# Performance work log

Measured on AMD Instinct MI355X. Metric: run time of the kernel, lower is better.

The kernel has to match this reference:

```python
import jax, jax.numpy as jnp
import numpy as np

B, T, D, U = 64, 512, 256, 512


def setup_inputs() -> dict:
    key = jax.random.key(0)
    ks = jax.random.split(key, 8)
    g = lambda k, shape: (jax.random.normal(k, shape, dtype=jnp.float32) * 0.05)
    return {
        "x": jax.random.normal(ks[0], (B, T, D), dtype=jnp.float32),
        "h0": jnp.zeros((B, U), jnp.float32),
        "c0": jnp.zeros((B, U), jnp.float32),
        "W_f_short": g(ks[1], (D + U, U)),
        "b_f_short": -jnp.ones((U,), jnp.float32),
        "W_f_long": g(ks[2], (D + U, U)),
        "b_f_long": jnp.ones((U,), jnp.float32),
        "W_alpha": g(ks[3], (D + U, U)),
        "b_alpha": jnp.zeros((U,), jnp.float32),
        "W_m": g(ks[4], (D + U, D)),
        "b_m": jnp.zeros((D,), jnp.float32),
        "W_C": g(ks[5], (D + U, U)),
        "b_C": jnp.zeros((U,), jnp.float32),
        "W_o": g(ks[6], (D + U, U)),
        "b_o": jnp.zeros((U,), jnp.float32),
    }


def reference(x, h0, c0, W_f_short, b_f_short, W_f_long, b_f_long,
              W_alpha, b_alpha, W_m, b_m, W_C, b_C, W_o, b_o):
    # Fuse the five matmuls that share the same input hx=[h_prev, x_t]
    # into one; W_C uses a different input (hxm) and stays separate.
    units = h0.shape[-1]
    d = x.shape[-1]
    W_cat = jnp.concatenate([W_f_short, W_f_long, W_alpha, W_o, W_m], axis=1)
    b_cat = jnp.concatenate([b_f_short, b_f_long, b_alpha, b_o, b_m], axis=0)
    splits = np.cumsum([units, units, units, units])[:-0 or None]

    def step(carry, x_t):
        h_prev, c_prev = carry
        hx = jnp.concatenate([h_prev, x_t], axis=-1)          # [B, U+D]
        gates = hx @ W_cat + b_cat                            # [B, 4U+D]
        f_short = jax.nn.sigmoid(gates[:, :units])
        f_long = jax.nn.sigmoid(gates[:, units:2 * units])
        alpha = jax.nn.sigmoid(gates[:, 2 * units:3 * units])
        o_t = jax.nn.sigmoid(gates[:, 3 * units:4 * units])
        m_t = jax.nn.sigmoid(gates[:, 4 * units:])            # [B, D]
        f_t = alpha * f_short + (1.0 - alpha) * f_long
        i_t = 1.0 - f_t
        mod_x = m_t * x_t
        hxm = jnp.concatenate([h_prev, mod_x], axis=-1)
        c_hat = jnp.tanh(hxm @ W_C + b_C)
        c_t = f_t * c_prev + i_t * c_hat
        h_t = o_t * jnp.tanh(c_t)
        return (h_t, c_t), h_t

    xs = jnp.swapaxes(x, 0, 1)                                # [T, B, D]
    (_, _), hs = jax.lax.scan(step, (h0, c0), xs)             # hs: [T, B, U]
    return jnp.swapaxes(hs, 0, 1)                             # [B, T, U]
```

## Files before the change

### kernel.cpp

```cpp
#include <hip/hip_runtime.h>
#include <hip/hip_fp16.h>
#include <math.h>

typedef _Float16 h2 __attribute__((ext_vector_type(2)));
typedef _Float16 h8 __attribute__((ext_vector_type(8)));
typedef float    f4 __attribute__((ext_vector_type(4)));
typedef unsigned short     u16;
typedef unsigned int       u32;
typedef unsigned long long u64;

#define BB 64
#define TT 512
#define DD 256
#define UU 512

#define NBLK 64
#define CPB  44
#define XPB  36
#define UPB  8
#define MPB  4
#define NJ   2816
#define NJX  2304

#define OFF_W1   0ull
#define OFF_W2   (OFF_W1 + 2816ull*512*2)
#define OFF_WX   (OFF_W2 + 512ull*256*2)
#define OFF_B1   (OFF_WX + 2304ull*256*2)
#define OFF_HB   (OFF_B1 + 2816ull*4)
#define OFF_MX   (OFF_HB + 64ull*512*2)
#define OFF_CTR  (OFF_MX + 64ull*256*2)
#define OFF_XPRE (OFF_CTR + 16400ull*4)
#define WS_FULL  (OFF_XPRE + 512ull*2304*64*2)

__device__ __forceinline__ float sigf(float v)     { return 1.0f / (1.0f + __expf(-v)); }
__device__ __forceinline__ float tanhfast(float v) { return 1.0f - 2.0f / (__expf(2.0f * v) + 1.0f); }

__device__ __forceinline__ void waitflags_wave(u32* base, u32 tgt, int lane) {
    u32 it = 0;
    for (;;) {
        u32 v = __hip_atomic_load(base + lane * 16, __ATOMIC_RELAXED, __HIP_MEMORY_SCOPE_AGENT);
        if (__ballot(v >= tgt) == ~0ull) break;
        __builtin_amdgcn_s_sleep(1);
        if (++it > 2000000u) break;
    }
    (void)__hip_atomic_load(base + lane * 16, __ATOMIC_ACQUIRE, __HIP_MEMORY_SCOPE_AGENT);
}

__device__ __forceinline__ int pk5(int g, int u) { return (u >> 3) * 44 + g * 8 + (u & 7); }
__device__ __forceinline__ int pkm(int d)        { return (d >> 2) * 44 + 40 + (d & 3); }

__global__ void repack_kernel(const float* __restrict__ Wfs, const float* __restrict__ Wfl,
                              const float* __restrict__ Wal, const float* __restrict__ Wm,
                              const float* __restrict__ WC,  const float* __restrict__ Wo,
                              const float* __restrict__ bfs, const float* __restrict__ bfl,
                              const float* __restrict__ bal, const float* __restrict__ bm,
                              const float* __restrict__ bC,  const float* __restrict__ bo,
                              _Float16* __restrict__ W1, _Float16* __restrict__ W2,
                              _Float16* __restrict__ WxT, float* __restrict__ b1,
                              u32* __restrict__ ctr)
{
    const int stride = gridDim.x * blockDim.x;
    const int idx = blockIdx.x * blockDim.x + threadIdx.x;

    for (int i = idx; i < 2816 * 512; i += stride) {
        int J = i >> 9, k = i & 511;
        int blk = J / 44, c = J - blk * 44;
        float v;
        if (c < 40) {
            int grp = c >> 3, u = blk * 8 + (c & 7);
            const float* Wg = (grp == 0) ? Wfs : (grp == 1) ? Wfl : (grp == 2) ? Wal : (grp == 3) ? Wo : WC;
            v = Wg[(size_t)k * 512 + u];
        } else {
            int d = blk * 4 + (c - 40);
            v = Wm[(size_t)k * 256 + d];
        }
        W1[i] = (_Float16)v;
    }
    for (int i = idx; i < 512 * 256; i += stride) {
        int u = i >> 8, dd = i & 255;
        W2[i] = (_Float16)WC[(size_t)(512 + dd) * 512 + u];
    }
    for (int i = idx; i < 2304 * 256; i += stride) {
        int Jx = i >> 8, k2 = i & 255;
        int blk = Jx / 36, lc = Jx - blk * 36;
        float v;
        if (lc < 32) {
            int grp = lc >> 3, u = blk * 8 + (lc & 7);
            const float* Wg = (grp == 0) ? Wfs : (grp == 1) ? Wfl : (grp == 2) ? Wal : Wo;
            v = Wg[(size_t)(512 + k2) * 512 + u];
        } else {
            int d = blk * 4 + (lc - 32);
            v = Wm[(size_t)(512 + k2) * 256 + d];
        }
        WxT[i] = (_Float16)v;
    }
    for (int J = idx; J < 2816; J += stride) {
        int blk = J / 44, c = J - blk * 44;
        float v;
        if (c < 40) {
            int grp = c >> 3, u = blk * 8 + (c & 7);
            v = (grp == 0) ? bfs[u] : (grp == 1) ? bfl[u] : (grp == 2) ? bal[u] : (grp == 3) ? bo[u] : bC[u];
        } else {
            v = bm[blk * 4 + (c - 40)];
        }
        b1[J] = v;
    }
    for (int i = idx; i < 16400; i += stride) ctr[i] = 0;
}

__global__ __launch_bounds__(256) void xpre_kernel(const float* __restrict__ x,
                                                   const _Float16* __restrict__ WxT,
                                                   _Float16* __restrict__ Xpre)
{
    __shared__ _Float16 As[128 * 32];
    __shared__ _Float16 Bs[128 * 32];

    const int tid  = threadIdx.x;
    const int lane = tid & 63;
    const int w    = tid >> 6;
    const int wm   = w >> 1, wn = w & 1;
    const int quad = lane >> 4, l16 = lane & 15;
    const int row0 = blockIdx.x * 128;
    const int n0   = blockIdx.y * 128;

    f4 acc[4][4];
    for (int i = 0; i < 4; ++i)
        for (int j = 0; j < 4; ++j)
            acc[i][j] = (f4){0.f, 0.f, 0.f, 0.f};

    for (int kt = 0; kt < 8; ++kt) {
        const int k0 = kt * 32;
        {
            int r  = tid >> 3;
            int cg = (tid & 7) * 4;
            for (int rr = r; rr < 128; rr += 32) {
                f4 v = *(const f4*)&x[(size_t)(row0 + rr) * 256 + k0 + cg];
                As[rr * 32 + cg + 0] = (_Float16)v.x;
                As[rr * 32 + cg + 1] = (_Float16)v.y;
                As[rr * 32 + cg + 2] = (_Float16)v.z;
                As[rr * 32 + cg + 3] = (_Float16)v.w;
            }
        }
        {
            int r   = tid & 127;
            int seg = (tid >> 7) * 16;
            const _Float16* src = &WxT[(size_t)(n0 + r) * 256 + k0 + seg];
            *(f4*)&Bs[r * 32 + seg]     = *(const f4*)src;
            *(f4*)&Bs[r * 32 + seg + 8] = *(const f4*)(src + 8);
        }
        __syncthreads();

        h8 af[4], bf[4];
#pragma unroll
        for (int f = 0; f < 4; ++f) {
            af[f] = *(const h8*)&As[(wm * 64 + f * 16 + l16) * 32 + quad * 8];
            bf[f] = *(const h8*)&Bs[(wn * 64 + f * 16 + l16) * 32 + quad * 8];
        }
#pragma unroll
        for (int fm = 0; fm < 4; ++fm)
#pragma unroll
            for (int fn = 0; fn < 4; ++fn)
                acc[fm][fn] = __builtin_amdgcn_mfma_f32_16x16x32_f16(af[fm], bf[fn], acc[fm][fn], 0, 0, 0);
        __syncthreads();
    }

#pragma unroll
    for (int fm = 0; fm < 4; ++fm)
#pragma unroll
        for (int fn = 0; fn < 4; ++fn)
#pragma unroll
            for (int r = 0; r < 4; ++r) {
                int rr = row0 + wm * 64 + fm * 16 + quad * 4 + r;
                int J  = n0 + wn * 64 + fn * 16 + l16;
                int b = rr >> 9, tt = rr & 511;
                Xpre[((size_t)tt * NJX + J) * 64 + b] = (_Float16)acc[fm][fn][r];
            }
}

__global__ __launch_bounds__(256, 1) void rnn_coop(
    const float* __restrict__ x, const float* __restrict__ h0, const float* __restrict__ c0,
    const _Float16* __restrict__ W1, const _Float16* __restrict__ W2,
    const float* __restrict__ b1, const _Float16* __restrict__ Xpre,
    _Float16* __restrict__ hbuf, _Float16* __restrict__ mxbuf, u32* __restrict__ ctr,
    float* __restrict__ out)
{
    __shared__ __align__(16) _Float16 sW1[48 * 512];
    __shared__ float sS[48 * 68];
    __shared__ float sF[8 * 64];
    __shared__ float sO[8 * 64];
    __shared__ float sCP[8 * 64];
    __shared__ float sC[8 * 64];
    __shared__ float sB1[44];

    const int tid  = threadIdx.x;
    const int blk  = blockIdx.x;
    const int lane = tid & 63;
    const int w    = tid >> 6;
    const int l16  = lane & 15;
    const int quad = lane >> 4;
    const int swz  = l16 & 7;
    const int br   = w * 16 + l16;

    u32* hflag  = ctr;
    u32* mxflag = ctr + 1024;

    for (int idx = tid; idx < 48 * 64; idx += 256) {
        int r = idx >> 6, j = idx & 63;
        h8 v = {};
        if (r < CPB) v = *(const h8*)(W1 + ((size_t)(blk * CPB + r) * 512 + j * 8));
        *(h8*)&sW1[(r * 64 + (j ^ (r & 7))) * 8] = v;
    }
    h8 af2[8];
#pragma unroll
    for (int ks = 0; ks < 8; ++ks) {
        af2[ks] = (h8){};
        if (l16 < 8)
            af2[ks] = *(const h8*)(W2 + (size_t)(blk * UPB + l16) * 256 + ks * 32 + quad * 8);
    }
    if (tid < CPB) sB1[tid] = b1[blk * CPB + tid];
    for (int idx = tid; idx < UPB * 64; idx += 256) {
        int u = idx >> 6, b = idx & 63;
        sC[u * 64 + b] = c0[b * UU + blk * UPB + u];
    }
    if (tid < 128) {
        int q = tid >> 6, b = tid & 63;
        _Float16 hp[4];
#pragma unroll
        for (int r = 0; r < 4; ++r) hp[r] = (_Float16)h0[b * UU + blk * UPB + q * 4 + r];
        u64 hq; __builtin_memcpy(&hq, hp, 8);
        __hip_atomic_store((u64*)(hbuf + (size_t)b * 512 + blk * UPB + q * 4), hq,
                           __ATOMIC_RELAXED, __HIP_MEMORY_SCOPE_AGENT);
    }
    __syncthreads();
    if (tid == 0)
        __hip_atomic_store(&hflag[blk * 16], 1u, __ATOMIC_RELAXED, __HIP_MEMORY_SCOPE_AGENT);

    for (int t = 0; t < TT; ++t) {
        const _Float16* xp = Xpre + ((size_t)t * NJX + blk * XPB) * 64;
        float pfs[2], pfl[2], pal[2], pov[2];
#pragma unroll
        for (int i = 0; i < 2; ++i) {
            int u = w * 2 + i;
            pfs[i] = (float)xp[(size_t)u * 64 + lane];
            pfl[i] = (float)xp[(size_t)(8 + u) * 64 + lane];
            pal[i] = (float)xp[(size_t)(16 + u) * 64 + lane];
            pov[i] = (float)xp[(size_t)(24 + u) * 64 + lane];
        }
        float pxm[4] = {0.f, 0.f, 0.f, 0.f};
        f4 pxv = {0.f, 0.f, 0.f, 0.f};
        if (quad == 2) {
#pragma unroll
            for (int r = 0; r < 4; ++r)
                pxm[r] = (float)xp[(size_t)(32 + r) * 64 + br];
            pxv = *(const f4*)&x[((size_t)br * TT + t) * DD + blk * MPB];
        }

        if (w == 0) waitflags_wave(hflag, (u32)(t + 1), lane);
        __syncthreads();

        h8 bf[16];
#pragma unroll
        for (int ks = 0; ks < 16; ++ks)
            bf[ks] = *(const h8*)(hbuf + (size_t)br * 512 + (ks * 4 + quad) * 8);

        f4 acc2 = {0.f, 0.f, 0.f, 0.f};
#pragma unroll
        for (int ks = 0; ks < 16; ++ks) {
            int jx = (ks * 4 + quad) ^ swz;
            h8 a2 = *(const h8*)&sW1[((32 + l16) * 64 + jx) * 8];
            acc2 = __builtin_amdgcn_mfma_f32_16x16x32_f16(a2, bf[ks], acc2, 0, 0, 0);
        }
        if (quad < 2) {
#pragma unroll
            for (int r = 0; r < 4; ++r)
                sS[(32 + quad * 4 + r) * 68 + br] = acc2[r];
        }
        if (quad == 2) {
            _Float16 mp[4];
#pragma unroll
            for (int r = 0; r < 4; ++r) {
                float mr = acc2[r] + sB1[40 + r] + pxm[r];
                mp[r] = (_Float16)(sigf(mr) * pxv[r]);
            }
            u64 mq; __builtin_memcpy(&mq, mp, 8);
            __hip_atomic_store((u64*)(mxbuf + (size_t)br * 256 + blk * MPB), mq,
                               __ATOMIC_RELAXED, __HIP_MEMORY_SCOPE_AGENT);
        }

        f4 acc0 = {0.f, 0.f, 0.f, 0.f}, acc1 = {0.f, 0.f, 0.f, 0.f};
#pragma unroll
        for (int ks = 0; ks < 16; ++ks) {
            int jx = (ks * 4 + quad) ^ swz;
            h8 a0 = *(const h8*)&sW1[((     l16) * 64 + jx) * 8];
            h8 a1 = *(const h8*)&sW1[((16 + l16) * 64 + jx) * 8];
            acc0 = __builtin_amdgcn_mfma_f32_16x16x32_f16(a0, bf[ks], acc0, 0, 0, 0);
            acc1 = __builtin_amdgcn_mfma_f32_16x16x32_f16(a1, bf[ks], acc1, 0, 0, 0);
        }
        asm volatile("s_waitcnt vmcnt(0)" ::: "memory");
        if (quad == 2 && l16 == 0)
            __hip_atomic_fetch_add(&mxflag[blk * 16], 1u, __ATOMIC_RELAXED, __HIP_MEMORY_SCOPE_AGENT);
#pragma unroll
        for (int r = 0; r < 4; ++r) {
            sS[(     quad * 4 + r) * 68 + br] = acc0[r];
            sS[(16 + quad * 4 + r) * 68 + br] = acc1[r];
        }
        __syncthreads();

#pragma unroll
        for (int i = 0; i < 2; ++i) {
            int u = w * 2 + i;
            float fs = sigf(sS[u * 68 + lane]        + sB1[u]      + pfs[i]);
            float fl = sigf(sS[(8 + u) * 68 + lane]  + sB1[8 + u]  + pfl[i]);
            float al = sigf(sS[(16 + u) * 68 + lane] + sB1[16 + u] + pal[i]);
            sF[u * 64 + lane]  = al * fs + (1.0f - al) * fl;
            sO[u * 64 + lane]  = sigf(sS[(24 + u) * 68 + lane] + sB1[24 + u] + pov[i]);
            sCP[u * 64 + lane] = sS[(32 + u) * 68 + lane] + sB1[32 + u];
        }
        __syncthreads();

        if (w == 0) waitflags_wave(mxflag, 4u * (u32)(t + 1), lane);
        __syncthreads();

        {
            h8 bf2[8];
#pragma unroll
            for (int ks = 0; ks < 8; ++ks)
                bf2[ks] = *(const h8*)(mxbuf + (size_t)br * 256 + (ks * 4 + quad) * 8);
            f4 aq = {0.f, 0.f, 0.f, 0.f};
#pragma unroll
            for (int ks = 0; ks < 8; ++ks)
                aq = __builtin_amdgcn_mfma_f32_16x16x32_f16(af2[ks], bf2[ks], aq, 0, 0, 0);

            f4 ovec = {0.f, 0.f, 0.f, 0.f};
            const int u0 = quad * 4;
            if (quad < 2) {
                float hv[4];
#pragma unroll
                for (int r = 0; r < 4; ++r) {
                    int u = u0 + r;
                    float ch = tanhfast(aq[r] + sCP[u * 64 + br]);
                    float f  = sF[u * 64 + br];
                    float c  = f * sC[u * 64 + br] + (1.0f - f) * ch;
                    sC[u * 64 + br] = c;
                    hv[r] = sO[u * 64 + br] * tanhfast(c);
                }
                _Float16 hp[4] = {(_Float16)hv[0], (_Float16)hv[1], (_Float16)hv[2], (_Float16)hv[3]};
                u64 hq; __builtin_memcpy(&hq, hp, 8);
                __hip_atomic_store((u64*)(hbuf + (size_t)br * 512 + blk * UPB + u0), hq,
                                   __ATOMIC_RELAXED, __HIP_MEMORY_SCOPE_AGENT);
                ovec = (f4){hv[0], hv[1], hv[2], hv[3]};
            }
            __syncthreads();
            if (tid == 0)
                __hip_atomic_store(&hflag[blk * 16], (u32)(t + 2), __ATOMIC_RELAXED, __HIP_MEMORY_SCOPE_AGENT);
            if (quad < 2)
                __builtin_nontemporal_store(ovec, (f4*)&out[((size_t)br * TT + t) * UU + blk * UPB + u0]);
        }
    }
}

__global__ __launch_bounds__(704) void rnn_fb(const float* __restrict__ x,
                                              const float* __restrict__ h0,
                                              const float* __restrict__ c0,
                                              const _Float16* __restrict__ W1,
                                              const _Float16* __restrict__ W2,
                                              const _Float16* __restrict__ WxT,
                                              const float* __restrict__ b1g,
                                              float* __restrict__ out)
{
    __shared__ float g_ld[2816];
    __shared__ float b1_ld[2816];
    __shared__ float h_ld[512];
    __shared__ float x_ld[256];
    __shared__ float f_ld[512];
    __shared__ float o_ld[512];
    __shared__ float c_ld[512];
    __shared__ __align__(16) h2 hx_h2[256];
    __shared__ __align__(16) h2 x16_h2[128];
    __shared__ __align__(16) h2 modx_h2[128];

    const int tid = threadIdx.x;
    const int b   = blockIdx.x;
    const int j0  = tid * 4;
    const int c   = j0 % 44;
    const bool hasx = (c < 32) || (c >= 40);
    const int Jx0 = (j0 / 44) * 36 + (c < 32 ? c : c - 8);

    for (int j = tid; j < 2816; j += 704) b1_ld[j] = b1g[j];
    if (tid < 512) {
        h_ld[tid] = h0[b * 512 + tid];
        c_ld[tid] = c0[b * 512 + tid];
    }
    __syncthreads();

    const f4* __restrict__ w1r = (const f4*)(W1 + (size_t)j0 * 512);
    const float* __restrict__ xrow = x + (size_t)b * TT * DD;
    float* __restrict__ orow = out + (size_t)b * TT * UU;

    for (int t = 0; t < TT; ++t) {
        if (tid < 256) {
            h2 p; p[0] = (_Float16)h_ld[2 * tid]; p[1] = (_Float16)h_ld[2 * tid + 1];
            hx_h2[tid] = p;
        } else if (tid < 384) {
            int i = tid - 256;
            float v0 = xrow[t * DD + 2 * i];
            float v1 = xrow[t * DD + 2 * i + 1];
            x_ld[2 * i] = v0; x_ld[2 * i + 1] = v1;
            h2 p; p[0] = (_Float16)v0; p[1] = (_Float16)v1;
            x16_h2[i] = p;
        }
        __syncthreads();

        float a0 = b1_ld[j0], a1 = b1_ld[j0 + 1], a2 = b1_ld[j0 + 2], a3 = b1_ld[j0 + 3];
        if (hasx) {
            const f4* xr0 = (const f4*)(WxT + (size_t)Jx0 * 256);
            const f4* xr1 = xr0 + 32;
            const f4* xr2 = xr0 + 64;
            const f4* xr3 = xr0 + 96;
            const f4* xv4 = (const f4*)x16_h2;
#pragma unroll 4
            for (int kc = 0; kc < 32; ++kc) {
                f4 xv = xv4[kc];
                f4 w0 = xr0[kc], w1 = xr1[kc], w2 = xr2[kc], w3 = xr3[kc];
                const h2* xpv = (const h2*)&xv;
                const h2* p0 = (const h2*)&w0; const h2* p1 = (const h2*)&w1;
                const h2* p2 = (const h2*)&w2; const h2* p3 = (const h2*)&w3;
#pragma unroll
                for (int u = 0; u < 4; ++u) {
                    a0 = __builtin_amdgcn_fdot2(p0[u], xpv[u], a0, false);
                    a1 = __builtin_amdgcn_fdot2(p1[u], xpv[u], a1, false);
                    a2 = __builtin_amdgcn_fdot2(p2[u], xpv[u], a2, false);
                    a3 = __builtin_amdgcn_fdot2(p3[u], xpv[u], a3, false);
                }
            }
        }
        {
            const f4* hx4 = (const f4*)hx_h2;
            const f4* r0 = w1r;
            const f4* r1 = w1r + 64;
            const f4* r2 = w1r + 128;
            const f4* r3 = w1r + 192;
#pragma unroll 4
            for (int kc = 0; kc < 64; ++kc) {
                f4 hv = hx4[kc];
                f4 w0 = r0[kc], w1 = r1[kc], w2 = r2[kc], w3 = r3[kc];
                const h2* hp = (const h2*)&hv;
                const h2* p0 = (const h2*)&w0; const h2* p1 = (const h2*)&w1;
                const h2* p2 = (const h2*)&w2; const h2* p3 = (const h2*)&w3;
#pragma unroll
                for (int u = 0; u < 4; ++u) {
                    a0 = __builtin_amdgcn_fdot2(p0[u], hp[u], a0, false);
                    a1 = __builtin_amdgcn_fdot2(p1[u], hp[u], a1, false);
                    a2 = __builtin_amdgcn_fdot2(p2[u], hp[u], a2, false);
                    a3 = __builtin_amdgcn_fdot2(p3[u], hp[u], a3, false);
                }
            }
        }
        g_ld[j0] = a0; g_ld[j0 + 1] = a1; g_ld[j0 + 2] = a2; g_ld[j0 + 3] = a3;
        __syncthreads();

        if (tid < 128) {
            float m0 = sigf(g_ld[pkm(2 * tid)]);
            float m1 = sigf(g_ld[pkm(2 * tid + 1)]);
            h2 p;
            p[0] = (_Float16)(m0 * x_ld[2 * tid]);
            p[1] = (_Float16)(m1 * x_ld[2 * tid + 1]);
            modx_h2[tid] = p;
        } else if (tid < 640) {
            int u = tid - 128;
            float fs = sigf(g_ld[pk5(0, u)]);
            float fl = sigf(g_ld[pk5(1, u)]);
            float al = sigf(g_ld[pk5(2, u)]);
            f_ld[u] = al * fs + (1.0f - al) * fl;
            o_ld[u] = sigf(g_ld[pk5(3, u)]);
        }
        __syncthreads();

        if (tid < 512) {
            float s = g_ld[pk5(4, tid)];
            const f4* w2r = (const f4*)(W2 + (size_t)tid * 256);
            const f4* mx4 = (const f4*)modx_h2;
#pragma unroll 4
            for (int kc = 0; kc < 32; ++kc) {
                f4 wv = w2r[kc];
                f4 mv = mx4[kc];
                const h2* wp = (const h2*)&wv;
                const h2* mp = (const h2*)&mv;
#pragma unroll
                for (int u = 0; u < 4; ++u)
                    s = __builtin_amdgcn_fdot2(wp[u], mp[u], s, false);
            }
            float ch = tanhfast(s);
            float f  = f_ld[tid];
            float cc = f * c_ld[tid] + (1.0f - f) * ch;
            c_ld[tid] = cc;
            float h  = o_ld[tid] * tanhfast(cc);
            h_ld[tid] = h;
            orow[t * UU + tid] = h;
        }
        __syncthreads();
    }
}

extern "C" void kernel_launch(void* const* d_in, const int* in_sizes, int n_in,
                              void* d_out, int out_size, void* d_ws, size_t ws_size,
                              hipStream_t stream)
{
    (void)in_sizes; (void)n_in; (void)out_size;
    const float* x   = (const float*)d_in[0];
    const float* h0  = (const float*)d_in[1];
    const float* c0  = (const float*)d_in[2];
    const float* Wfs = (const float*)d_in[3];
    const float* bfs = (const float*)d_in[4];
    const float* Wfl = (const float*)d_in[5];
    const float* bfl = (const float*)d_in[6];
    const float* Wal = (const float*)d_in[7];
    const float* bal = (const float*)d_in[8];
    const float* Wm  = (const float*)d_in[9];
    const float* bm  = (const float*)d_in[10];
    const float* WC  = (const float*)d_in[11];
    const float* bC  = (const float*)d_in[12];
    const float* Wo  = (const float*)d_in[13];
    const float* bo  = (const float*)d_in[14];

    char* ws = (char*)d_ws;
    _Float16* W1   = (_Float16*)(ws + OFF_W1);
    _Float16* W2   = (_Float16*)(ws + OFF_W2);
    _Float16* WxT  = (_Float16*)(ws + OFF_WX);
    float*    b1   = (float*)   (ws + OFF_B1);
    _Float16* hbuf = (_Float16*)(ws + OFF_HB);
    _Float16* mxbf = (_Float16*)(ws + OFF_MX);
    u32*      ctr  = (u32*)     (ws + OFF_CTR);
    _Float16* Xpre = (_Float16*)(ws + OFF_XPRE);

    repack_kernel<<<dim3(1024), dim3(256), 0, stream>>>(
        Wfs, Wfl, Wal, Wm, WC, Wo, bfs, bfl, bal, bm, bC, bo, W1, W2, WxT, b1, ctr);

    if (ws_size >= WS_FULL) {
        xpre_kernel<<<dim3(256, 18), dim3(256), 0, stream>>>(x, WxT, Xpre);
        rnn_coop<<<dim3(NBLK), dim3(256), 0, stream>>>(
            x, h0, c0, W1, W2, b1, Xpre, hbuf, mxbf, ctr, (float*)d_out);
    } else {
        rnn_fb<<<dim3(BB), dim3(704), 0, stream>>>(
            x, h0, c0, W1, W2, WxT, b1, (float*)d_out);
    }
}
```

Baseline: 4.258 ms.

## Replace per-block flag barriers with tagged value records for cross-block exchange

Each h and m*x value pair is now stored as a 64-bit record that carries a timestep tag, so consumer threads poll the data itself instead of waiting on per-block counters and then reading. This drops the flag stores, fetch-adds, vmcnt waits and the extra block-wide barriers around each wait, cutting latency on the serial timestep chain. In exchange each exchange buffer is four times larger, every thread spins on its own records with more global traffic, and correctness depends on the 64-bit atomic stores being seen whole.

```diff
diff --git a/kernel.cpp b/kernel.cpp
--- a/kernel.cpp
+++ b/kernel.cpp
@@ -27,23 +27,20 @@
 #define OFF_WX   (OFF_W2 + 512ull*256*2)
 #define OFF_B1   (OFF_WX + 2304ull*256*2)
 #define OFF_HB   (OFF_B1 + 2816ull*4)
-#define OFF_MX   (OFF_HB + 64ull*512*2)
-#define OFF_CTR  (OFF_MX + 64ull*256*2)
+#define OFF_MX   (OFF_HB + 64ull*256*8)
+#define OFF_CTR  (OFF_MX + 64ull*128*8)
 #define OFF_XPRE (OFF_CTR + 16400ull*4)
 #define WS_FULL  (OFF_XPRE + 512ull*2304*64*2)
 
 __device__ __forceinline__ float sigf(float v)     { return 1.0f / (1.0f + __expf(-v)); }
 __device__ __forceinline__ float tanhfast(float v) { return 1.0f - 2.0f / (__expf(2.0f * v) + 1.0f); }
 
-__device__ __forceinline__ void waitflags_wave(u32* base, u32 tgt, int lane) {
-    u32 it = 0;
-    for (;;) {
-        u32 v = __hip_atomic_load(base + lane * 16, __ATOMIC_RELAXED, __HIP_MEMORY_SCOPE_AGENT);
-        if (__ballot(v >= tgt) == ~0ull) break;
-        __builtin_amdgcn_s_sleep(1);
-        if (++it > 2000000u) break;
-    }
-    (void)__hip_atomic_load(base + lane * 16, __ATOMIC_ACQUIRE, __HIP_MEMORY_SCOPE_AGENT);
+__device__ __forceinline__ u64 pack_rec(float a, float b, u32 tag) {
+    _Float16 ha = (_Float16)a, hb = (_Float16)b;
+    u16 ua, ub;
+    __builtin_memcpy(&ua, &ha, 2);
+    __builtin_memcpy(&ub, &hb, 2);
+    return (u64)((u32)ua | ((u32)ub << 16)) | ((u64)tag << 32);
 }
 
 __device__ __forceinline__ int pk5(int g, int u) { return (u >> 3) * 44 + g * 8 + (u & 7); }
@@ -57,7 +54,7 @@
                               const float* __restrict__ bC,  const float* __restrict__ bo,
                               _Float16* __restrict__ W1, _Float16* __restrict__ W2,
                               _Float16* __restrict__ WxT, float* __restrict__ b1,
-                              u32* __restrict__ ctr)
+                              u64* __restrict__ recs)
 {
     const int stride = gridDim.x * blockDim.x;
     const int idx = blockIdx.x * blockDim.x + threadIdx.x;
@@ -105,7 +102,7 @@
         }
         b1[J] = v;
     }
-    for (int i = idx; i < 16400; i += stride) ctr[i] = 0;
+    for (int i = idx; i < 24576; i += stride) recs[i] = 0ull;
 }
 
 __global__ __launch_bounds__(256) void xpre_kernel(const float* __restrict__ x,
@@ -150,17 +147,17 @@
         }
         __syncthreads();
 
-        h8 af[4], bf[4];
+        h8 af[4], bfr[4];
 #pragma unroll
         for (int f = 0; f < 4; ++f) {
-            af[f] = *(const h8*)&As[(wm * 64 + f * 16 + l16) * 32 + quad * 8];
-            bf[f] = *(const h8*)&Bs[(wn * 64 + f * 16 + l16) * 32 + quad * 8];
+            af[f]  = *(const h8*)&As[(wm * 64 + f * 16 + l16) * 32 + quad * 8];
+            bfr[f] = *(const h8*)&Bs[(wn * 64 + f * 16 + l16) * 32 + quad * 8];
         }
 #pragma unroll
         for (int fm = 0; fm < 4; ++fm)
 #pragma unroll
             for (int fn = 0; fn < 4; ++fn)
-                acc[fm][fn] = __builtin_amdgcn_mfma_f32_16x16x32_f16(af[fm], bf[fn], acc[fm][fn], 0, 0, 0);
+                acc[fm][fn] = __builtin_amdgcn_mfma_f32_16x16x32_f16(af[fm], bfr[fn], acc[fm][fn], 0, 0, 0);
         __syncthreads();
     }
 
@@ -181,7 +178,7 @@
     const float* __restrict__ x, const float* __restrict__ h0, const float* __restrict__ c0,
     const _Float16* __restrict__ W1, const _Float16* __restrict__ W2,
     const float* __restrict__ b1, const _Float16* __restrict__ Xpre,
-    _Float16* __restrict__ hbuf, _Float16* __restrict__ mxbuf, u32* __restrict__ ctr,
+    u64* __restrict__ hbufT, u64* __restrict__ mxbufT,
     float* __restrict__ out)
 {
     __shared__ __align__(16) _Float16 sW1[48 * 512];
@@ -201,9 +198,6 @@
     const int swz  = l16 & 7;
     const int br   = w * 16 + l16;
 
-    u32* hflag  = ctr;
-    u32* mxflag = ctr + 1024;
-
     for (int idx = tid; idx < 48 * 64; idx += 256) {
         int r = idx >> 6, j = idx & 63;
         h8 v = {};
@@ -224,16 +218,16 @@
     }
     if (tid < 128) {
         int q = tid >> 6, b = tid & 63;
-        _Float16 hp[4];
-#pragma unroll
-        for (int r = 0; r < 4; ++r) hp[r] = (_Float16)h0[b * UU + blk * UPB + q * 4 + r];
-        u64 hq; __builtin_memcpy(&hq, hp, 8);
-        __hip_atomic_store((u64*)(hbuf + (size_t)b * 512 + blk * UPB + q * 4), hq,
+        float v0 = h0[b * UU + blk * UPB + q * 4 + 0];
+        float v1 = h0[b * UU + blk * UPB + q * 4 + 1];
+        float v2 = h0[b * UU + blk * UPB + q * 4 + 2];
+        float v3 = h0[b * UU + blk * UPB + q * 4 + 3];
+        __hip_atomic_store(hbufT + (size_t)b * 256 + blk * 4 + q * 2 + 0, pack_rec(v0, v1, 1u),
                            __ATOMIC_RELAXED, __HIP_MEMORY_SCOPE_AGENT);
+        __hip_atomic_store(hbufT + (size_t)b * 256 + blk * 4 + q * 2 + 1, pack_rec(v2, v3, 1u),
+                           __ATOMIC_RELAXED, __HIP_MEMORY_SCOPE_AGENT);
     }
     __syncthreads();
-    if (tid == 0)
-        __hip_atomic_store(&hflag[blk * 16], 1u, __ATOMIC_RELAXED, __HIP_MEMORY_SCOPE_AGENT);
 
     for (int t = 0; t < TT; ++t) {
         const _Float16* xp = Xpre + ((size_t)t * NJX + blk * XPB) * 64;
@@ -255,13 +249,35 @@
             pxv = *(const f4*)&x[((size_t)br * TT + t) * DD + blk * MPB];
         }
 
-        if (w == 0) waitflags_wave(hflag, (u32)(t + 1), lane);
-        __syncthreads();
-
+        u64 rec[16][4];
+        {
+            u64* hT = hbufT + (size_t)br * 256;
+            const u32 expt = (u32)t + 1u;
+            bool ok; u32 guard = 0;
+            do {
+#pragma unroll
+                for (int ks = 0; ks < 16; ++ks) {
+                    const int base = (ks * 4 + quad) * 4;
+#pragma unroll
+                    for (int j = 0; j < 4; ++j)
+                        rec[ks][j] = __hip_atomic_load(hT + base + j,
+                                                       __ATOMIC_RELAXED, __HIP_MEMORY_SCOPE_AGENT);
+                }
+                ok = true;
+#pragma unroll
+                for (int ks = 0; ks < 16; ++ks)
+#pragma unroll
+                    for (int j = 0; j < 4; ++j)
+                        ok = ok && ((u32)(rec[ks][j] >> 32) == expt);
+                if (!ok) __builtin_amdgcn_s_sleep(1);
+            } while (!ok && ++guard < 2000000u);
+        }
         h8 bf[16];
 #pragma unroll
-        for (int ks = 0; ks < 16; ++ks)
-            bf[ks] = *(const h8*)(hbuf + (size_t)br * 512 + (ks * 4 + quad) * 8);
+        for (int ks = 0; ks < 16; ++ks) {
+            u32 d[4] = {(u32)rec[ks][0], (u32)rec[ks][1], (u32)rec[ks][2], (u32)rec[ks][3]};
+            __builtin_memcpy(&bf[ks], d, 16);
+        }
 
         f4 acc2 = {0.f, 0.f, 0.f, 0.f};
 #pragma unroll
@@ -276,15 +292,14 @@
                 sS[(32 + quad * 4 + r) * 68 + br] = acc2[r];
         }
         if (quad == 2) {
-            _Float16 mp[4];
-#pragma unroll
-            for (int r = 0; r < 4; ++r) {
-                float mr = acc2[r] + sB1[40 + r] + pxm[r];
-                mp[r] = (_Float16)(sigf(mr) * pxv[r]);
-            }
-            u64 mq; __builtin_memcpy(&mq, mp, 8);
-            __hip_atomic_store((u64*)(mxbuf + (size_t)br * 256 + blk * MPB), mq,
-                               __ATOMIC_RELAXED, __HIP_MEMORY_SCOPE_AGENT);
+            const u32 tagm = (u32)t + 1u;
+#pragma unroll
+            for (int p = 0; p < 2; ++p) {
+                float m0 = sigf(acc2[2 * p]     + sB1[40 + 2 * p]     + pxm[2 * p])     * pxv[2 * p];
+                float m1 = sigf(acc2[2 * p + 1] + sB1[40 + 2 * p + 1] + pxm[2 * p + 1]) * pxv[2 * p + 1];
+                __hip_atomic_store(mxbufT + (size_t)br * 128 + blk * 2 + p, pack_rec(m0, m1, tagm),
+                                   __ATOMIC_RELAXED, __HIP_MEMORY_SCOPE_AGENT);
+            }
         }
 
         f4 acc0 = {0.f, 0.f, 0.f, 0.f}, acc1 = {0.f, 0.f, 0.f, 0.f};
@@ -296,9 +311,6 @@
             acc0 = __builtin_amdgcn_mfma_f32_16x16x32_f16(a0, bf[ks], acc0, 0, 0, 0);
             acc1 = __builtin_amdgcn_mfma_f32_16x16x32_f16(a1, bf[ks], acc1, 0, 0, 0);
         }
-        asm volatile("s_waitcnt vmcnt(0)" ::: "memory");
-        if (quad == 2 && l16 == 0)
-            __hip_atomic_fetch_add(&mxflag[blk * 16], 1u, __ATOMIC_RELAXED, __HIP_MEMORY_SCOPE_AGENT);
 #pragma unroll
         for (int r = 0; r < 4; ++r) {
             sS[(     quad * 4 + r) * 68 + br] = acc0[r];
@@ -318,22 +330,40 @@
         }
         __syncthreads();
 
-        if (w == 0) waitflags_wave(mxflag, 4u * (u32)(t + 1), lane);
-        __syncthreads();
-
+        u64 rec2[8][4];
         {
-            h8 bf2[8];
-#pragma unroll
-            for (int ks = 0; ks < 8; ++ks)
-                bf2[ks] = *(const h8*)(mxbuf + (size_t)br * 256 + (ks * 4 + quad) * 8);
+            u64* mT = mxbufT + (size_t)br * 128;
+            const u32 expt = (u32)t + 1u;
+            bool ok; u32 guard = 0;
+            do {
+#pragma unroll
+                for (int ks = 0; ks < 8; ++ks) {
+                    const int base = (ks * 4 + quad) * 4;
+#pragma unroll
+                    for (int j = 0; j < 4; ++j)
+                        rec2[ks][j] = __hip_atomic_load(mT + base + j,
+                                                        __ATOMIC_RELAXED, __HIP_MEMORY_SCOPE_AGENT);
+                }
+                ok = true;
+#pragma unroll
+                for (int ks = 0; ks < 8; ++ks)
+#pragma unroll
+                    for (int j = 0; j < 4; ++j)
+                        ok = ok && ((u32)(rec2[ks][j] >> 32) == expt);
+                if (!ok) __builtin_amdgcn_s_sleep(1);
+            } while (!ok && ++guard < 2000000u);
+        }
+
+        {
             f4 aq = {0.f, 0.f, 0.f, 0.f};
 #pragma unroll
-            for (int ks = 0; ks < 8; ++ks)
-                aq = __builtin_amdgcn_mfma_f32_16x16x32_f16(af2[ks], bf2[ks], aq, 0, 0, 0);
-
-            f4 ovec = {0.f, 0.f, 0.f, 0.f};
-            const int u0 = quad * 4;
+            for (int ks = 0; ks < 8; ++ks) {
+                u32 d[4] = {(u32)rec2[ks][0], (u32)rec2[ks][1], (u32)rec2[ks][2], (u32)rec2[ks][3]};
+                h8 bf2; __builtin_memcpy(&bf2, d, 16);
+                aq = __builtin_amdgcn_mfma_f32_16x16x32_f16(af2[ks], bf2, aq, 0, 0, 0);
+            }
             if (quad < 2) {
+                const int u0 = quad * 4;
                 float hv[4];
 #pragma unroll
                 for (int r = 0; r < 4; ++r) {
@@ -344,17 +374,16 @@
                     sC[u * 64 + br] = c;
                     hv[r] = sO[u * 64 + br] * tanhfast(c);
                 }
-                _Float16 hp[4] = {(_Float16)hv[0], (_Float16)hv[1], (_Float16)hv[2], (_Float16)hv[3]};
-                u64 hq; __builtin_memcpy(&hq, hp, 8);
-                __hip_atomic_store((u64*)(hbuf + (size_t)br * 512 + blk * UPB + u0), hq,
+                const u32 tagh = (u32)t + 2u;
+                __hip_atomic_store(hbufT + (size_t)br * 256 + blk * 4 + quad * 2 + 0,
+                                   pack_rec(hv[0], hv[1], tagh),
                                    __ATOMIC_RELAXED, __HIP_MEMORY_SCOPE_AGENT);
-                ovec = (f4){hv[0], hv[1], hv[2], hv[3]};
-            }
-            __syncthreads();
-            if (tid == 0)
-                __hip_atomic_store(&hflag[blk * 16], (u32)(t + 2), __ATOMIC_RELAXED, __HIP_MEMORY_SCOPE_AGENT);
-            if (quad < 2)
+                __hip_atomic_store(hbufT + (size_t)br * 256 + blk * 4 + quad * 2 + 1,
+                                   pack_rec(hv[2], hv[3], tagh),
+                                   __ATOMIC_RELAXED, __HIP_MEMORY_SCOPE_AGENT);
+                f4 ovec = {hv[0], hv[1], hv[2], hv[3]};
                 __builtin_nontemporal_store(ovec, (f4*)&out[((size_t)br * TT + t) * UU + blk * UPB + u0]);
+            }
         }
     }
 }
@@ -528,18 +557,17 @@
     _Float16* W2   = (_Float16*)(ws + OFF_W2);
     _Float16* WxT  = (_Float16*)(ws + OFF_WX);
     float*    b1   = (float*)   (ws + OFF_B1);
-    _Float16* hbuf = (_Float16*)(ws + OFF_HB);
-    _Float16* mxbf = (_Float16*)(ws + OFF_MX);
-    u32*      ctr  = (u32*)     (ws + OFF_CTR);
+    u64*      hbT  = (u64*)     (ws + OFF_HB);
+    u64*      mxT  = (u64*)     (ws + OFF_MX);
     _Float16* Xpre = (_Float16*)(ws + OFF_XPRE);
 
     repack_kernel<<<dim3(1024), dim3(256), 0, stream>>>(
-        Wfs, Wfl, Wal, Wm, WC, Wo, bfs, bfl, bal, bm, bC, bo, W1, W2, WxT, b1, ctr);
+        Wfs, Wfl, Wal, Wm, WC, Wo, bfs, bfl, bal, bm, bC, bo, W1, W2, WxT, b1, hbT);
 
     if (ws_size >= WS_FULL) {
         xpre_kernel<<<dim3(256, 18), dim3(256), 0, stream>>>(x, WxT, Xpre);
         rnn_coop<<<dim3(NBLK), dim3(256), 0, stream>>>(
-            x, h0, c0, W1, W2, b1, Xpre, hbuf, mxbf, ctr, (float*)d_out);
+            x, h0, c0, W1, W2, b1, Xpre, hbT, mxT, (float*)d_out);
     } else {
         rnn_fb<<<dim3(BB), dim3(704), 0, stream>>>(
             x, h0, c0, W1, W2, WxT, b1, (float*)d_out);
```

After: 11.94 ms. 180% more time.

## Replace block-wide barriers with per-wave flag planes and register-resident gate math

Applied to the files above, without the earlier changes.

Each wave now handles its own batch slice end to end. It waits on per-wave flag planes (one per batch quarter) instead of going through wave-0 polling plus __syncthreads. Gate activations are computed in registers using cross-lane shuffles rather than staging through shared memory, and the cell state stays in registers. The mod-x flag becomes a per-wave store of the step index instead of an atomic counter, and the spin timeout is doubled. This removes several block barriers and LDS round trips per timestep from the serial recurrence, at the cost of more flag traffic (four planes) and more per-wave polling.

```diff
diff --git a/kernel.cpp b/kernel.cpp
--- a/kernel.cpp
+++ b/kernel.cpp
@@ -35,13 +35,13 @@
 __device__ __forceinline__ float sigf(float v)     { return 1.0f / (1.0f + __expf(-v)); }
 __device__ __forceinline__ float tanhfast(float v) { return 1.0f - 2.0f / (__expf(2.0f * v) + 1.0f); }
 
-__device__ __forceinline__ void waitflags_wave(u32* base, u32 tgt, int lane) {
+__device__ __forceinline__ void plane_wait(u32* base, u32 tgt, int lane) {
     u32 it = 0;
     for (;;) {
         u32 v = __hip_atomic_load(base + lane * 16, __ATOMIC_RELAXED, __HIP_MEMORY_SCOPE_AGENT);
         if (__ballot(v >= tgt) == ~0ull) break;
         __builtin_amdgcn_s_sleep(1);
-        if (++it > 2000000u) break;
+        if (++it > 4000000u) break;
     }
     (void)__hip_atomic_load(base + lane * 16, __ATOMIC_ACQUIRE, __HIP_MEMORY_SCOPE_AGENT);
 }
@@ -150,17 +150,17 @@
         }
         __syncthreads();
 
-        h8 af[4], bf[4];
+        h8 af[4], bfr[4];
 #pragma unroll
         for (int f = 0; f < 4; ++f) {
-            af[f] = *(const h8*)&As[(wm * 64 + f * 16 + l16) * 32 + quad * 8];
-            bf[f] = *(const h8*)&Bs[(wn * 64 + f * 16 + l16) * 32 + quad * 8];
+            af[f]  = *(const h8*)&As[(wm * 64 + f * 16 + l16) * 32 + quad * 8];
+            bfr[f] = *(const h8*)&Bs[(wn * 64 + f * 16 + l16) * 32 + quad * 8];
         }
 #pragma unroll
         for (int fm = 0; fm < 4; ++fm)
 #pragma unroll
             for (int fn = 0; fn < 4; ++fn)
-                acc[fm][fn] = __builtin_amdgcn_mfma_f32_16x16x32_f16(af[fm], bf[fn], acc[fm][fn], 0, 0, 0);
+                acc[fm][fn] = __builtin_amdgcn_mfma_f32_16x16x32_f16(af[fm], bfr[fn], acc[fm][fn], 0, 0, 0);
         __syncthreads();
     }
 
@@ -185,24 +185,16 @@
     float* __restrict__ out)
 {
     __shared__ __align__(16) _Float16 sW1[48 * 512];
-    __shared__ float sS[48 * 68];
-    __shared__ float sF[8 * 64];
-    __shared__ float sO[8 * 64];
-    __shared__ float sCP[8 * 64];
-    __shared__ float sC[8 * 64];
     __shared__ float sB1[44];
 
     const int tid  = threadIdx.x;
     const int blk  = blockIdx.x;
     const int lane = tid & 63;
-    const int w    = tid >> 6;
+    const int q    = tid >> 6;
     const int l16  = lane & 15;
     const int quad = lane >> 4;
     const int swz  = l16 & 7;
-    const int br   = w * 16 + l16;
-
-    u32* hflag  = ctr;
-    u32* mxflag = ctr + 1024;
+    const int br   = q * 16 + l16;
 
     for (int idx = tid; idx < 48 * 64; idx += 256) {
         int r = idx >> 6, j = idx & 63;
@@ -218,45 +210,51 @@
             af2[ks] = *(const h8*)(W2 + (size_t)(blk * UPB + l16) * 256 + ks * 32 + quad * 8);
     }
     if (tid < CPB) sB1[tid] = b1[blk * CPB + tid];
-    for (int idx = tid; idx < UPB * 64; idx += 256) {
-        int u = idx >> 6, b = idx & 63;
-        sC[u * 64 + b] = c0[b * UU + blk * UPB + u];
+    float cr[4] = {0.f, 0.f, 0.f, 0.f};
+    if (quad < 2) {
+#pragma unroll
+        for (int r = 0; r < 4; ++r)
+            cr[r] = c0[(size_t)br * UU + blk * UPB + quad * 4 + r];
     }
     if (tid < 128) {
-        int q = tid >> 6, b = tid & 63;
+        int qq = tid >> 6, b = tid & 63;
         _Float16 hp[4];
 #pragma unroll
-        for (int r = 0; r < 4; ++r) hp[r] = (_Float16)h0[b * UU + blk * UPB + q * 4 + r];
+        for (int r = 0; r < 4; ++r) hp[r] = (_Float16)h0[(size_t)b * UU + blk * UPB + qq * 4 + r];
         u64 hq; __builtin_memcpy(&hq, hp, 8);
-        __hip_atomic_store((u64*)(hbuf + (size_t)b * 512 + blk * UPB + q * 4), hq,
+        __hip_atomic_store((u64*)(hbuf + (size_t)b * 512 + blk * UPB + qq * 4), hq,
                            __ATOMIC_RELAXED, __HIP_MEMORY_SCOPE_AGENT);
     }
     __syncthreads();
-    if (tid == 0)
-        __hip_atomic_store(&hflag[blk * 16], 1u, __ATOMIC_RELAXED, __HIP_MEMORY_SCOPE_AGENT);
+    if (tid < 4)
+        __hip_atomic_store(&ctr[(tid * 64 + blk) * 16], 1u,
+                           __ATOMIC_RELAXED, __HIP_MEMORY_SCOPE_AGENT);
+
+    u32* hfl = ctr + (size_t)q * 1024;
+    u32* mfl = ctr + 4096 + (size_t)q * 1024;
 
     for (int t = 0; t < TT; ++t) {
-        const _Float16* xp = Xpre + ((size_t)t * NJX + blk * XPB) * 64;
-        float pfs[2], pfl[2], pal[2], pov[2];
-#pragma unroll
-        for (int i = 0; i < 2; ++i) {
-            int u = w * 2 + i;
-            pfs[i] = (float)xp[(size_t)u * 64 + lane];
-            pfl[i] = (float)xp[(size_t)(8 + u) * 64 + lane];
-            pal[i] = (float)xp[(size_t)(16 + u) * 64 + lane];
-            pov[i] = (float)xp[(size_t)(24 + u) * 64 + lane];
-        }
+        float pfs[4], pflv[4], pal[4], pov[4];
         float pxm[4] = {0.f, 0.f, 0.f, 0.f};
         f4 pxv = {0.f, 0.f, 0.f, 0.f};
-        if (quad == 2) {
-#pragma unroll
-            for (int r = 0; r < 4; ++r)
-                pxm[r] = (float)xp[(size_t)(32 + r) * 64 + br];
+        if (quad < 2) {
+            const _Float16* xp = Xpre + ((size_t)t * NJX + blk * XPB) * 64 + br;
+#pragma unroll
+            for (int r = 0; r < 4; ++r) {
+                int u = quad * 4 + r;
+                pfs[r]  = (float)xp[(size_t)u * 64];
+                pflv[r] = (float)xp[(size_t)(8 + u) * 64];
+                pal[r]  = (float)xp[(size_t)(16 + u) * 64];
+                pov[r]  = (float)xp[(size_t)(24 + u) * 64];
+            }
+        } else if (quad == 2) {
+            const _Float16* xq = Xpre + ((size_t)t * NJX + blk * XPB + 32) * 64 + br;
+#pragma unroll
+            for (int r = 0; r < 4; ++r) pxm[r] = (float)xq[(size_t)r * 64];
             pxv = *(const f4*)&x[((size_t)br * TT + t) * DD + blk * MPB];
         }
 
-        if (w == 0) waitflags_wave(hflag, (u32)(t + 1), lane);
-        __syncthreads();
+        plane_wait(hfl, (u32)t + 1u, lane);
 
         h8 bf[16];
 #pragma unroll
@@ -269,11 +267,6 @@
             int jx = (ks * 4 + quad) ^ swz;
             h8 a2 = *(const h8*)&sW1[((32 + l16) * 64 + jx) * 8];
             acc2 = __builtin_amdgcn_mfma_f32_16x16x32_f16(a2, bf[ks], acc2, 0, 0, 0);
-        }
-        if (quad < 2) {
-#pragma unroll
-            for (int r = 0; r < 4; ++r)
-                sS[(32 + quad * 4 + r) * 68 + br] = acc2[r];
         }
         if (quad == 2) {
             _Float16 mp[4];
@@ -298,64 +291,60 @@
         }
         asm volatile("s_waitcnt vmcnt(0)" ::: "memory");
         if (quad == 2 && l16 == 0)
-            __hip_atomic_fetch_add(&mxflag[blk * 16], 1u, __ATOMIC_RELAXED, __HIP_MEMORY_SCOPE_AGENT);
+            __hip_atomic_store(&mfl[blk * 16], (u32)t + 1u,
+                               __ATOMIC_RELAXED, __HIP_MEMORY_SCOPE_AGENT);
+
+        float fv[4], ov[4], cpv[4];
 #pragma unroll
         for (int r = 0; r < 4; ++r) {
-            sS[(     quad * 4 + r) * 68 + br] = acc0[r];
-            sS[(16 + quad * 4 + r) * 68 + br] = acc1[r];
-        }
-        __syncthreads();
-
-#pragma unroll
-        for (int i = 0; i < 2; ++i) {
-            int u = w * 2 + i;
-            float fs = sigf(sS[u * 68 + lane]        + sB1[u]      + pfs[i]);
-            float fl = sigf(sS[(8 + u) * 68 + lane]  + sB1[8 + u]  + pfl[i]);
-            float al = sigf(sS[(16 + u) * 68 + lane] + sB1[16 + u] + pal[i]);
-            sF[u * 64 + lane]  = al * fs + (1.0f - al) * fl;
-            sO[u * 64 + lane]  = sigf(sS[(24 + u) * 68 + lane] + sB1[24 + u] + pov[i]);
-            sCP[u * 64 + lane] = sS[(32 + u) * 68 + lane] + sB1[32 + u];
-        }
-        __syncthreads();
-
-        if (w == 0) waitflags_wave(mxflag, 4u * (u32)(t + 1), lane);
-        __syncthreads();
-
-        {
-            h8 bf2[8];
-#pragma unroll
-            for (int ks = 0; ks < 8; ++ks)
-                bf2[ks] = *(const h8*)(mxbuf + (size_t)br * 256 + (ks * 4 + quad) * 8);
-            f4 aq = {0.f, 0.f, 0.f, 0.f};
-#pragma unroll
-            for (int ks = 0; ks < 8; ++ks)
-                aq = __builtin_amdgcn_mfma_f32_16x16x32_f16(af2[ks], bf2[ks], aq, 0, 0, 0);
-
-            f4 ovec = {0.f, 0.f, 0.f, 0.f};
-            const int u0 = quad * 4;
+            float flsh = __shfl_xor(acc0[r], 32);
+            float osh  = __shfl_xor(acc1[r], 32);
             if (quad < 2) {
-                float hv[4];
-#pragma unroll
-                for (int r = 0; r < 4; ++r) {
-                    int u = u0 + r;
-                    float ch = tanhfast(aq[r] + sCP[u * 64 + br]);
-                    float f  = sF[u * 64 + br];
-                    float c  = f * sC[u * 64 + br] + (1.0f - f) * ch;
-                    sC[u * 64 + br] = c;
-                    hv[r] = sO[u * 64 + br] * tanhfast(c);
-                }
-                _Float16 hp[4] = {(_Float16)hv[0], (_Float16)hv[1], (_Float16)hv[2], (_Float16)hv[3]};
-                u64 hq; __builtin_memcpy(&hq, hp, 8);
-                __hip_atomic_store((u64*)(hbuf + (size_t)br * 512 + blk * UPB + u0), hq,
-                                   __ATOMIC_RELAXED, __HIP_MEMORY_SCOPE_AGENT);
-                ovec = (f4){hv[0], hv[1], hv[2], hv[3]};
-            }
-            __syncthreads();
-            if (tid == 0)
-                __hip_atomic_store(&hflag[blk * 16], (u32)(t + 2), __ATOMIC_RELAXED, __HIP_MEMORY_SCOPE_AGENT);
-            if (quad < 2)
-                __builtin_nontemporal_store(ovec, (f4*)&out[((size_t)br * TT + t) * UU + blk * UPB + u0]);
-        }
+                int u = quad * 4 + r;
+                float fs = sigf(acc0[r] + sB1[u]      + pfs[r]);
+                float fl = sigf(flsh    + sB1[8 + u]  + pflv[r]);
+                float al = sigf(acc1[r] + sB1[16 + u] + pal[r]);
+                fv[r]  = al * fs + (1.0f - al) * fl;
+                ov[r]  = sigf(osh + sB1[24 + u] + pov[r]);
+                cpv[r] = acc2[r] + sB1[32 + u];
+            }
+        }
+
+        plane_wait(mfl, (u32)t + 1u, lane);
+
+        h8 bf2[8];
+#pragma unroll
+        for (int ks = 0; ks < 8; ++ks)
+            bf2[ks] = *(const h8*)(mxbuf + (size_t)br * 256 + (ks * 4 + quad) * 8);
+        f4 aq = {0.f, 0.f, 0.f, 0.f};
+#pragma unroll
+        for (int ks = 0; ks < 8; ++ks)
+            aq = __builtin_amdgcn_mfma_f32_16x16x32_f16(af2[ks], bf2[ks], aq, 0, 0, 0);
+
+        f4 ovec = {0.f, 0.f, 0.f, 0.f};
+        if (quad < 2) {
+            float hv[4];
+#pragma unroll
+            for (int r = 0; r < 4; ++r) {
+                float ch = tanhfast(aq[r] + cpv[r]);
+                float f  = fv[r];
+                float c  = f * cr[r] + (1.0f - f) * ch;
+                cr[r] = c;
+                hv[r] = ov[r] * tanhfast(c);
+            }
+            _Float16 hp[4] = {(_Float16)hv[0], (_Float16)hv[1], (_Float16)hv[2], (_Float16)hv[3]};
+            u64 hq; __builtin_memcpy(&hq, hp, 8);
+            __hip_atomic_store((u64*)(hbuf + (size_t)br * 512 + blk * UPB + quad * 4), hq,
+                               __ATOMIC_RELAXED, __HIP_MEMORY_SCOPE_AGENT);
+            ovec = (f4){hv[0], hv[1], hv[2], hv[3]};
+        }
+        asm volatile("s_waitcnt vmcnt(0)" ::: "memory");
+        if (lane == 0)
+            __hip_atomic_store(&hfl[blk * 16], (u32)t + 2u,
+                               __ATOMIC_RELAXED, __HIP_MEMORY_SCOPE_AGENT);
+        if (quad < 2)
+            __builtin_nontemporal_store(ovec,
+                (f4*)&out[((size_t)br * TT + t) * UU + blk * UPB + quad * 4]);
     }
 }
 
```

Result: slower. 4.485 ms (+5.3%).
